# Optimization experiments

Measured on AMD Instinct MI355X. Metric: run time of the kernel, lower is better.

## Reference

```python
import jax, jax.numpy as jnp
import numpy as np


def _tsallis15_probs(x):
    """entmax-1.5 / Tsallis alpha=1.5 mapping over axis=1. x: [n, d] logits."""
    x = (x - jnp.max(x, axis=1, keepdims=True)) * 0.5
    xs = -jnp.sort(-x, axis=1)                       # descending sort  [n, d]
    d = x.shape[1]
    rho = jnp.arange(1, d + 1, dtype=x.dtype)        # 1..d
    mean = jnp.cumsum(xs, axis=1) / rho
    mean_sq = jnp.cumsum(xs * xs, axis=1) / rho
    ss = rho * (mean_sq - mean * mean)
    delta = (1.0 - ss) / rho
    tau = mean - jnp.sqrt(jnp.clip(delta, 0.0))
    support_size = jnp.sum(tau <= xs, axis=1)        # [n]
    tau_star = jnp.take_along_axis(tau, (support_size - 1)[:, None], axis=1)
    y = jnp.clip(x - tau_star, 0.0)
    return y * y                                     # p*, rows sum to 1


def setup_inputs() -> dict:
    key = jax.random.key(0)
    k1, k2 = jax.random.split(key)
    inp = jax.random.normal(k1, (2048, 32000), dtype=jnp.float32)
    target = jax.random.randint(k2, (2048,), 0, 32000, dtype=jnp.int64)
    return {"input": inp, "target": target}


def reference(input, target):
    n = input.shape[0]
    p_star = _tsallis15_probs(input)
    # omega_tsallis15: (1 - sum p^{3/2}) / 0.75 per row
    loss = (1.0 - jnp.sum(p_star * jnp.sqrt(p_star), axis=1)) / 0.75
    # scatter_add(-1) at the target class, then <p* - e_y, x> per row
    pm = p_star.at[jnp.arange(n), target].add(-1.0)
    loss = loss + jnp.einsum('ij,ij->i', pm, input)
    # reduction='elementwise_mean', ignore_index=-100 (<0: no masking)
    return jnp.sum(loss) / n
```

## Files before the change

### kernel.cpp

```cpp
#include <hip/hip_runtime.h>
#include <math.h>

#define BLOCK 512
#define NV 16
#define NWAVES (BLOCK / 64)
#define CAND_CAP 6144
#define NREG 12

__device__ __forceinline__ float waveReduceMax(float v) {
#pragma unroll
    for (int off = 32; off > 0; off >>= 1)
        v = fmaxf(v, __shfl_down(v, off, 64));
    return v;
}
__device__ __forceinline__ float waveReduceSum(float v) {
#pragma unroll
    for (int off = 32; off > 0; off >>= 1)
        v += __shfl_down(v, off, 64);
    return v;
}

__global__ __launch_bounds__(BLOCK, 4) void tsallis15_kernel(
    const float* __restrict__ x, const int* __restrict__ tgt,
    float* __restrict__ out, int n, int d, float inv_n)
{
    __shared__ float s_cand[CAND_CAP];
    __shared__ float s_red[NWAVES];
    __shared__ int   s_cnt;
    __shared__ float s_bcast;

    const int row  = blockIdx.x;
    const int t    = threadIdx.x;
    const int lane = t & 63;
    const int wave = t >> 6;
    const float* __restrict__ xr = x + (size_t)row * (size_t)d;

    if (t == 0) s_cnt = 0;

    float4 r[NV];
#pragma unroll
    for (int i = 0; i < NV; ++i) {
        int e = (i * BLOCK + t) * 4;
        if (e + 4 <= d) {
            r[i] = *reinterpret_cast<const float4*>(xr + e);
        } else {
            float4 v = make_float4(-INFINITY, -INFINITY, -INFINITY, -INFINITY);
            if (e < d)     v.x = xr[e];
            if (e + 1 < d) v.y = xr[e + 1];
            if (e + 2 < d) v.z = xr[e + 2];
            r[i] = v;
        }
    }

    float m = -INFINITY;
#pragma unroll
    for (int i = 0; i < NV; ++i)
        m = fmaxf(m, fmaxf(fmaxf(r[i].x, r[i].y), fmaxf(r[i].z, r[i].w)));
    m = waveReduceMax(m);
    if (lane == 0) s_red[wave] = m;
    __syncthreads();
    if (wave == 0) {
        float v = (lane < NWAVES) ? s_red[lane] : -INFINITY;
        v = waveReduceMax(v);
        if (lane == 0) s_bcast = v;
    }
    __syncthreads();
    const float rowmax = s_bcast;

    const float thr = rowmax - 2.0f;
#pragma unroll
    for (int i = 0; i < NV; ++i) {
        float vals[4] = { r[i].x, r[i].y, r[i].z, r[i].w };
#pragma unroll
        for (int c = 0; c < 4; ++c) {
            float v = vals[c];
            bool pred = (v >= thr);
            unsigned long long mask = __ballot(pred);
            if (mask) {
                int base;
                if (lane == 0) base = atomicAdd(&s_cnt, __popcll(mask));
                base = __shfl(base, 0, 64);
                if (pred) {
                    int pos = base + (int)__popcll(mask & ((1ull << lane) - 1ull));
                    if (pos < CAND_CAP) s_cand[pos] = (v - rowmax) * 0.5f;
                }
            }
        }
    }
    __syncthreads();

    if (wave == 0) {
        const float xt = (lane == 0) ? xr[tgt[row]] : 0.0f;

        const int k = min(s_cnt, CAND_CAP);

        float ur[NREG];
#pragma unroll
        for (int j = 0; j < NREG; ++j) {
            int idx = lane + 64 * j;
            ur[j] = (idx < k) ? s_cand[idx] : -1e30f;
        }

        float lo = -1.0f, hi = 0.0f;
        for (int it = 0; it < 18; ++it) {
            float tau = 0.5f * (lo + hi);
            float acc = 0.0f;
#pragma unroll
            for (int j = 0; j < NREG; ++j) {
                float u = ur[j] - tau;
                acc += (u > 0.0f) ? u * u : 0.0f;
            }
            for (int j = 64 * NREG + lane; j < k; j += 64) {
                float u = s_cand[j] - tau;
                if (u > 0.0f) acc += u * u;
            }
            float tot = waveReduceSum(acc);
            tot = __shfl(tot, 0, 64);
            if (tot >= 1.0f) lo = tau; else hi = tau;
        }
        const float tau_b = 0.5f * (lo + hi);

        float s1 = 0.0f, s2 = 0.0f, sc = 0.0f;
#pragma unroll
        for (int j = 0; j < NREG; ++j) {
            float u = ur[j];
            if (u > tau_b) { s1 += u; s2 += u * u; sc += 1.0f; }
        }
        for (int j = 64 * NREG + lane; j < k; j += 64) {
            float u = s_cand[j];
            if (u > tau_b) { s1 += u; s2 += u * u; sc += 1.0f; }
        }
        s1 = waveReduceSum(s1); s1 = __shfl(s1, 0, 64);
        s2 = waveReduceSum(s2); s2 = __shfl(s2, 0, 64);
        sc = waveReduceSum(sc); sc = __shfl(sc, 0, 64);
        float mean  = s1 / sc;
        float ss    = s2 - s1 * mean;
        float delta = (1.0f - ss) / sc;
        if (delta < 0.0f) delta = 0.0f;
        const float tau_star = mean - sqrtf(delta);

        float p32 = 0.0f, dot = 0.0f;
#pragma unroll
        for (int j = 0; j < NREG; ++j) {
            float u = ur[j] - tau_star;
            if (u > 0.0f) {
                float p = u * u;
                p32 += p * u;
                dot += p * (2.0f * ur[j] + rowmax);
            }
        }
        for (int j = 64 * NREG + lane; j < k; j += 64) {
            float uc = s_cand[j];
            float u  = uc - tau_star;
            if (u > 0.0f) {
                float p = u * u;
                p32 += p * u;
                dot += p * (2.0f * uc + rowmax);
            }
        }
        p32 = waveReduceSum(p32);
        dot = waveReduceSum(dot);
        if (lane == 0) {
            float loss = (1.0f - p32) * (4.0f / 3.0f) + dot - xt;
            atomicAdd(out, loss * inv_n);
        }
    }
}

extern "C" void kernel_launch(void* const* d_in, const int* in_sizes, int n_in,
                              void* d_out, int out_size, void* d_ws, size_t ws_size,
                              hipStream_t stream) {
    const float* x   = (const float*)d_in[0];
    const int*   tgt = (const int*)d_in[1];
    float*       out = (float*)d_out;

    const int n = in_sizes[1];
    const int d = in_sizes[0] / n;

    hipMemsetAsync(out, 0, (size_t)out_size * sizeof(float), stream);
    tsallis15_kernel<<<n, BLOCK, 0, stream>>>(x, tgt, out, n, d, 1.0f / (float)n);
}
```

Measured before the change: 381.1 us.

## Stream row in chunks with per-wave running-max candidate filtering to cut registers

Instead of holding all 64 row values per thread in registers until the block max is known, each wave loads four float4 chunks at a time, tracks a running wave max, and appends values within 2 of it to a per-wave shared segment, pruning the segment when it fills. After the block max is known, the surviving candidates are filtered again into a final list, with a fallback that rereads the row from global memory if any wave's segment overflowed. This lowers register pressure so launch bounds can be raised to 6 blocks per CU. The cost is more shared memory (about 48KB per block, which may itself limit occupancy), extra ballot work, and a possible second global read on overflow.

```diff
diff --git a/kernel.cpp b/kernel.cpp
--- a/kernel.cpp
+++ b/kernel.cpp
@@ -2,15 +2,16 @@
 #include <math.h>
 
 #define BLOCK 512
+#define NWAVES (BLOCK / 64)
 #define NV 16
-#define NWAVES (BLOCK / 64)
-#define CAND_CAP 6144
+#define SEGCAP 1024
+#define FCAP 4096
 #define NREG 12
 
-__device__ __forceinline__ float waveReduceMax(float v) {
-#pragma unroll
-    for (int off = 32; off > 0; off >>= 1)
-        v = fmaxf(v, __shfl_down(v, off, 64));
+__device__ __forceinline__ float waveAllMax(float v) {
+#pragma unroll
+    for (int off = 1; off < 64; off <<= 1)
+        v = fmaxf(v, __shfl_xor(v, off, 64));
     return v;
 }
 __device__ __forceinline__ float waveReduceSum(float v) {
@@ -20,13 +21,32 @@
     return v;
 }
 
-__global__ __launch_bounds__(BLOCK, 4) void tsallis15_kernel(
+__device__ __forceinline__ int wavePrune(float* seg, int cnt, float thr, int lane) {
+    int newcnt = 0;
+    for (int base = 0; base < cnt; base += 64) {
+        int idx = base + lane;
+        bool valid = idx < cnt;
+        float v = valid ? seg[idx] : -INFINITY;
+        bool keep = valid && (v >= thr);
+        unsigned long long mask = __ballot(keep);
+        if (keep) {
+            int pos = newcnt + (int)__popcll(mask & ((1ull << lane) - 1ull));
+            seg[pos] = v;
+        }
+        newcnt += (int)__popcll(mask);
+    }
+    return newcnt;
+}
+
+__global__ __launch_bounds__(BLOCK, 6) void tsallis15_kernel(
     const float* __restrict__ x, const int* __restrict__ tgt,
     float* __restrict__ out, int n, int d, float inv_n)
 {
-    __shared__ float s_cand[CAND_CAP];
+    __shared__ float s_seg[NWAVES][SEGCAP];
+    __shared__ float s_final[FCAP];
     __shared__ float s_red[NWAVES];
-    __shared__ int   s_cnt;
+    __shared__ int   s_fcnt;
+    __shared__ int   s_flag;
     __shared__ float s_bcast;
 
     const int row  = blockIdx.x;
@@ -35,54 +55,114 @@
     const int wave = t >> 6;
     const float* __restrict__ xr = x + (size_t)row * (size_t)d;
 
-    if (t == 0) s_cnt = 0;
-
-    float4 r[NV];
-#pragma unroll
-    for (int i = 0; i < NV; ++i) {
-        int e = (i * BLOCK + t) * 4;
-        if (e + 4 <= d) {
-            r[i] = *reinterpret_cast<const float4*>(xr + e);
-        } else {
-            float4 v = make_float4(-INFINITY, -INFINITY, -INFINITY, -INFINITY);
-            if (e < d)     v.x = xr[e];
-            if (e + 1 < d) v.y = xr[e + 1];
-            if (e + 2 < d) v.z = xr[e + 2];
-            r[i] = v;
-        }
-    }
-
-    float m = -INFINITY;
-#pragma unroll
-    for (int i = 0; i < NV; ++i)
-        m = fmaxf(m, fmaxf(fmaxf(r[i].x, r[i].y), fmaxf(r[i].z, r[i].w)));
-    m = waveReduceMax(m);
-    if (lane == 0) s_red[wave] = m;
+    if (t == 0) { s_fcnt = 0; s_flag = 0; }
+
+    float* seg = &s_seg[wave][0];
+    float wmax = -INFINITY;
+    int   cnt  = 0;
+    bool  ovf  = false;
+
+    for (int i0 = 0; i0 < NV; i0 += 4) {
+        float4 c[4];
+#pragma unroll
+        for (int q = 0; q < 4; ++q) {
+            int e = ((i0 + q) * BLOCK + t) * 4;
+            if (e + 4 <= d) {
+                c[q] = *reinterpret_cast<const float4*>(xr + e);
+            } else {
+                float4 v = make_float4(-INFINITY, -INFINITY, -INFINITY, -INFINITY);
+                if (e < d)     v.x = xr[e];
+                if (e + 1 < d) v.y = xr[e + 1];
+                if (e + 2 < d) v.z = xr[e + 2];
+                c[q] = v;
+            }
+        }
+        float m = -INFINITY;
+#pragma unroll
+        for (int q = 0; q < 4; ++q)
+            m = fmaxf(m, fmaxf(fmaxf(c[q].x, c[q].y), fmaxf(c[q].z, c[q].w)));
+        wmax = fmaxf(wmax, waveAllMax(m));
+        const float thr = wmax - 2.0f;
+#pragma unroll
+        for (int q = 0; q < 4; ++q) {
+            float vals[4] = { c[q].x, c[q].y, c[q].z, c[q].w };
+#pragma unroll
+            for (int s = 0; s < 4; ++s) {
+                float v = vals[s];
+                bool pred = (v >= thr);
+                unsigned long long mask = __ballot(pred);
+                if (mask) {
+                    int pc = (int)__popcll(mask);
+                    if (cnt + pc > SEGCAP) {
+                        cnt = wavePrune(seg, cnt, thr, lane);
+                        if (cnt + pc > SEGCAP) ovf = true;
+                    }
+                    if (!ovf) {
+                        if (pred) {
+                            int pos = cnt + (int)__popcll(mask & ((1ull << lane) - 1ull));
+                            seg[pos] = v;
+                        }
+                        cnt += pc;
+                    }
+                }
+            }
+        }
+    }
+
+    if (lane == 0) {
+        s_red[wave] = wmax;
+        if (ovf) s_flag = 1;
+    }
     __syncthreads();
     if (wave == 0) {
         float v = (lane < NWAVES) ? s_red[lane] : -INFINITY;
-        v = waveReduceMax(v);
+        v = waveAllMax(v);
         if (lane == 0) s_bcast = v;
     }
     __syncthreads();
     const float rowmax = s_bcast;
-
-    const float thr = rowmax - 2.0f;
-#pragma unroll
-    for (int i = 0; i < NV; ++i) {
-        float vals[4] = { r[i].x, r[i].y, r[i].z, r[i].w };
-#pragma unroll
-        for (int c = 0; c < 4; ++c) {
-            float v = vals[c];
-            bool pred = (v >= thr);
-            unsigned long long mask = __ballot(pred);
+    const float thrF   = rowmax - 2.0f;
+
+    if (s_flag == 0) {
+        for (int base = 0; base < cnt; base += 64) {
+            int idx = base + lane;
+            float v = (idx < cnt) ? seg[idx] : -INFINITY;
+            bool keep = (v >= thrF);
+            unsigned long long mask = __ballot(keep);
             if (mask) {
-                int base;
-                if (lane == 0) base = atomicAdd(&s_cnt, __popcll(mask));
-                base = __shfl(base, 0, 64);
-                if (pred) {
-                    int pos = base + (int)__popcll(mask & ((1ull << lane) - 1ull));
-                    if (pos < CAND_CAP) s_cand[pos] = (v - rowmax) * 0.5f;
+                int bpos;
+                if (lane == 0) bpos = atomicAdd(&s_fcnt, (int)__popcll(mask));
+                bpos = __shfl(bpos, 0, 64);
+                if (keep) {
+                    int pos = bpos + (int)__popcll(mask & ((1ull << lane) - 1ull));
+                    if (pos < FCAP) s_final[pos] = (v - rowmax) * 0.5f;
+                }
+            }
+        }
+    } else {
+        for (int i = 0; i < NV; ++i) {
+            int e = (i * BLOCK + t) * 4;
+            float4 c = make_float4(-INFINITY, -INFINITY, -INFINITY, -INFINITY);
+            if (e + 4 <= d) c = *reinterpret_cast<const float4*>(xr + e);
+            else {
+                if (e < d)     c.x = xr[e];
+                if (e + 1 < d) c.y = xr[e + 1];
+                if (e + 2 < d) c.z = xr[e + 2];
+            }
+            float vals[4] = { c.x, c.y, c.z, c.w };
+#pragma unroll
+            for (int s = 0; s < 4; ++s) {
+                float v = vals[s];
+                bool keep = (v >= thrF);
+                unsigned long long mask = __ballot(keep);
+                if (mask) {
+                    int bpos;
+                    if (lane == 0) bpos = atomicAdd(&s_fcnt, (int)__popcll(mask));
+                    bpos = __shfl(bpos, 0, 64);
+                    if (keep) {
+                        int pos = bpos + (int)__popcll(mask & ((1ull << lane) - 1ull));
+                        if (pos < FCAP) s_final[pos] = (v - rowmax) * 0.5f;
+                    }
                 }
             }
         }
@@ -92,13 +172,13 @@
     if (wave == 0) {
         const float xt = (lane == 0) ? xr[tgt[row]] : 0.0f;
 
-        const int k = min(s_cnt, CAND_CAP);
+        const int k = min(s_fcnt, FCAP);
 
         float ur[NREG];
 #pragma unroll
         for (int j = 0; j < NREG; ++j) {
             int idx = lane + 64 * j;
-            ur[j] = (idx < k) ? s_cand[idx] : -1e30f;
+            ur[j] = (idx < k) ? s_final[idx] : -1e30f;
         }
 
         float lo = -1.0f, hi = 0.0f;
@@ -111,7 +191,7 @@
                 acc += (u > 0.0f) ? u * u : 0.0f;
             }
             for (int j = 64 * NREG + lane; j < k; j += 64) {
-                float u = s_cand[j] - tau;
+                float u = s_final[j] - tau;
                 if (u > 0.0f) acc += u * u;
             }
             float tot = waveReduceSum(acc);
@@ -127,7 +207,7 @@
             if (u > tau_b) { s1 += u; s2 += u * u; sc += 1.0f; }
         }
         for (int j = 64 * NREG + lane; j < k; j += 64) {
-            float u = s_cand[j];
+            float u = s_final[j];
             if (u > tau_b) { s1 += u; s2 += u * u; sc += 1.0f; }
         }
         s1 = waveReduceSum(s1); s1 = __shfl(s1, 0, 64);
@@ -150,7 +230,7 @@
             }
         }
         for (int j = 64 * NREG + lane; j < k; j += 64) {
-            float uc = s_cand[j];
+            float uc = s_final[j];
             float u  = uc - tau_star;
             if (u > 0.0f) {
                 float p = u * u;
```

Measured after the change: 384.9 us. Within noise of the previous version (+1.0%).

## Split each row across eight slice blocks with a two-kernel filter and solve

Applied to the files above, without the earlier changes.

Replaces the single one-block-per-row kernel with two kernels. The first uses eight blocks per row; each computes its slice max and writes the values above slicemax-2 to workspace. The second merges the slice candidates against the global row threshold, falling back to a full-row rescan if any slice overflows, and then runs the existing bisection solve. The aim is more blocks and higher occupancy for the memory-bound pass, at the cost of a second launch and workspace traffic.

```diff
diff --git a/kernel.cpp b/kernel.cpp
--- a/kernel.cpp
+++ b/kernel.cpp
@@ -1,11 +1,13 @@
 #include <hip/hip_runtime.h>
 #include <math.h>
 
-#define BLOCK 512
-#define NV 16
-#define NWAVES (BLOCK / 64)
-#define CAND_CAP 6144
-#define NREG 12
+#define SLICES     8
+#define SLICE_CAP  512
+#define K1_BLOCK   256
+#define K2_BLOCK   256
+#define MAXNI      8
+#define FCAP       6144
+#define NREG       12
 
 __device__ __forceinline__ float waveReduceMax(float v) {
 #pragma unroll
@@ -20,69 +22,179 @@
     return v;
 }
 
-__global__ __launch_bounds__(BLOCK, 4) void tsallis15_kernel(
-    const float* __restrict__ x, const int* __restrict__ tgt,
-    float* __restrict__ out, int n, int d, float inv_n)
+__global__ __launch_bounds__(K1_BLOCK, 4) void k1_filter(
+    const float* __restrict__ x, float* __restrict__ cand,
+    int* __restrict__ cnt, float* __restrict__ smax,
+    int d, int slice_len, int ni)
 {
-    __shared__ float s_cand[CAND_CAP];
-    __shared__ float s_red[NWAVES];
+    __shared__ float s_red[K1_BLOCK / 64];
     __shared__ int   s_cnt;
+    __shared__ float s_c[SLICE_CAP];
+    __shared__ float s_bmax;
+
+    const int sid  = blockIdx.x;
+    const int row  = sid >> 3;
+    const int sl   = sid & 7;
+    const int t    = threadIdx.x;
+    const int lane = t & 63;
+    const int wave = t >> 6;
+
+    if (t == 0) s_cnt = 0;
+
+    const int sbeg = sl * slice_len;
+    const int send = min(sbeg + slice_len, d);
+    const float* __restrict__ xr = x + (size_t)row * (size_t)d;
+
+    float4 c[MAXNI];
+#pragma unroll
+    for (int i = 0; i < MAXNI; ++i)
+        c[i] = make_float4(-INFINITY, -INFINITY, -INFINITY, -INFINITY);
+
+    float m = -INFINITY;
+    for (int i = 0; i < ni; ++i) {
+        int p = sbeg + (i * K1_BLOCK + t) * 4;
+        float4 v = make_float4(-INFINITY, -INFINITY, -INFINITY, -INFINITY);
+        if (p + 4 <= send) {
+            v = *reinterpret_cast<const float4*>(xr + p);
+        } else if (p < send) {
+            v.x = xr[p];
+            if (p + 1 < send) v.y = xr[p + 1];
+            if (p + 2 < send) v.z = xr[p + 2];
+        }
+        if (i < MAXNI) c[i] = v;
+        m = fmaxf(m, fmaxf(fmaxf(v.x, v.y), fmaxf(v.z, v.w)));
+    }
+    m = waveReduceMax(m);
+    if (lane == 0) s_red[wave] = m;
+    __syncthreads();
+    if (t == 0) {
+        float v = s_red[0];
+#pragma unroll
+        for (int w = 1; w < K1_BLOCK / 64; ++w) v = fmaxf(v, s_red[w]);
+        s_bmax = v;
+    }
+    __syncthreads();
+    const float mx  = s_bmax;
+    const float thr = mx - 2.0f;
+
+    for (int i = 0; i < ni; ++i) {
+        float4 v;
+        if (i < MAXNI) {
+            v = c[i];
+        } else {
+            int p = sbeg + (i * K1_BLOCK + t) * 4;
+            v = make_float4(-INFINITY, -INFINITY, -INFINITY, -INFINITY);
+            if (p + 4 <= send) v = *reinterpret_cast<const float4*>(xr + p);
+            else if (p < send) {
+                v.x = xr[p];
+                if (p + 1 < send) v.y = xr[p + 1];
+                if (p + 2 < send) v.z = xr[p + 2];
+            }
+        }
+        float vals[4] = { v.x, v.y, v.z, v.w };
+#pragma unroll
+        for (int s = 0; s < 4; ++s) {
+            float w = vals[s];
+            bool pred = (w >= thr);
+            unsigned long long mask = __ballot(pred);
+            if (mask) {
+                int base;
+                if (lane == 0) base = atomicAdd(&s_cnt, (int)__popcll(mask));
+                base = __shfl(base, 0, 64);
+                if (pred) {
+                    int pos = base + (int)__popcll(mask & ((1ull << lane) - 1ull));
+                    if (pos < SLICE_CAP) s_c[pos] = w;
+                }
+            }
+        }
+    }
+    __syncthreads();
+
+    const int total = s_cnt;
+    if (t == 0) { cnt[sid] = total; smax[sid] = mx; }
+    const int wr = min(total, SLICE_CAP);
+    for (int j = t; j < wr; j += K1_BLOCK)
+        cand[(size_t)sid * SLICE_CAP + j] = s_c[j];
+}
+
+__global__ __launch_bounds__(K2_BLOCK, 4) void k2_solve(
+    const float* __restrict__ x, const float* __restrict__ cand,
+    const int* __restrict__ cnt, const float* __restrict__ smax,
+    const int* __restrict__ tgt, float* __restrict__ out,
+    int d, float inv_n)
+{
+    __shared__ float s_final[FCAP];
+    __shared__ int   s_cnt8[SLICES];
+    __shared__ int   s_fcnt;
+    __shared__ int   s_ovf;
     __shared__ float s_bcast;
 
     const int row  = blockIdx.x;
     const int t    = threadIdx.x;
     const int lane = t & 63;
     const int wave = t >> 6;
+
+    if (t == 0) { s_fcnt = 0; s_ovf = 0; }
+
+    if (wave == 0) {
+        float v = -INFINITY;
+        if (lane < SLICES) {
+            int c8 = cnt[row * SLICES + lane];
+            s_cnt8[lane] = min(c8, SLICE_CAP);
+            if (c8 > SLICE_CAP) s_ovf = 1;
+            v = smax[row * SLICES + lane];
+        }
+#pragma unroll
+        for (int off = 1; off < SLICES; off <<= 1)
+            v = fmaxf(v, __shfl_xor(v, off, 64));
+        if (lane == 0) s_bcast = v;
+    }
+    __syncthreads();
+    const float rowmax = s_bcast;
+    const float thr    = rowmax - 2.0f;
     const float* __restrict__ xr = x + (size_t)row * (size_t)d;
 
-    if (t == 0) s_cnt = 0;
-
-    float4 r[NV];
-#pragma unroll
-    for (int i = 0; i < NV; ++i) {
-        int e = (i * BLOCK + t) * 4;
-        if (e + 4 <= d) {
-            r[i] = *reinterpret_cast<const float4*>(xr + e);
-        } else {
-            float4 v = make_float4(-INFINITY, -INFINITY, -INFINITY, -INFINITY);
-            if (e < d)     v.x = xr[e];
-            if (e + 1 < d) v.y = xr[e + 1];
-            if (e + 2 < d) v.z = xr[e + 2];
-            r[i] = v;
-        }
-    }
-
-    float m = -INFINITY;
-#pragma unroll
-    for (int i = 0; i < NV; ++i)
-        m = fmaxf(m, fmaxf(fmaxf(r[i].x, r[i].y), fmaxf(r[i].z, r[i].w)));
-    m = waveReduceMax(m);
-    if (lane == 0) s_red[wave] = m;
-    __syncthreads();
-    if (wave == 0) {
-        float v = (lane < NWAVES) ? s_red[lane] : -INFINITY;
-        v = waveReduceMax(v);
-        if (lane == 0) s_bcast = v;
-    }
-    __syncthreads();
-    const float rowmax = s_bcast;
-
-    const float thr = rowmax - 2.0f;
-#pragma unroll
-    for (int i = 0; i < NV; ++i) {
-        float vals[4] = { r[i].x, r[i].y, r[i].z, r[i].w };
-#pragma unroll
-        for (int c = 0; c < 4; ++c) {
-            float v = vals[c];
-            bool pred = (v >= thr);
-            unsigned long long mask = __ballot(pred);
+    if (!s_ovf) {
+        const float* __restrict__ cr = cand + (size_t)row * SLICES * SLICE_CAP;
+        for (int j = t; j < SLICES * SLICE_CAP; j += K2_BLOCK) {
+            int slice = j >> 9;
+            int pos   = j & (SLICE_CAP - 1);
+            float v   = cr[j];
+            bool keep = (pos < s_cnt8[slice]) && (v >= thr);
+            unsigned long long mask = __ballot(keep);
             if (mask) {
                 int base;
-                if (lane == 0) base = atomicAdd(&s_cnt, __popcll(mask));
+                if (lane == 0) base = atomicAdd(&s_fcnt, (int)__popcll(mask));
                 base = __shfl(base, 0, 64);
-                if (pred) {
-                    int pos = base + (int)__popcll(mask & ((1ull << lane) - 1ull));
-                    if (pos < CAND_CAP) s_cand[pos] = (v - rowmax) * 0.5f;
+                if (keep) {
+                    int p2 = base + (int)__popcll(mask & ((1ull << lane) - 1ull));
+                    if (p2 < FCAP) s_final[p2] = (v - rowmax) * 0.5f;
+                }
+            }
+        }
+    } else {
+        for (int e0 = t * 4; e0 < d; e0 += K2_BLOCK * 4) {
+            float4 v = make_float4(-INFINITY, -INFINITY, -INFINITY, -INFINITY);
+            if (e0 + 4 <= d) v = *reinterpret_cast<const float4*>(xr + e0);
+            else {
+                v.x = xr[e0];
+                if (e0 + 1 < d) v.y = xr[e0 + 1];
+                if (e0 + 2 < d) v.z = xr[e0 + 2];
+            }
+            float vals[4] = { v.x, v.y, v.z, v.w };
+#pragma unroll
+            for (int s = 0; s < 4; ++s) {
+                float w = vals[s];
+                bool keep = (w >= thr);
+                unsigned long long mask = __ballot(keep);
+                if (mask) {
+                    int base;
+                    if (lane == 0) base = atomicAdd(&s_fcnt, (int)__popcll(mask));
+                    base = __shfl(base, 0, 64);
+                    if (keep) {
+                        int p2 = base + (int)__popcll(mask & ((1ull << lane) - 1ull));
+                        if (p2 < FCAP) s_final[p2] = (w - rowmax) * 0.5f;
+                    }
                 }
             }
         }
@@ -92,13 +204,13 @@
     if (wave == 0) {
         const float xt = (lane == 0) ? xr[tgt[row]] : 0.0f;
 
-        const int k = min(s_cnt, CAND_CAP);
+        const int k = min(s_fcnt, FCAP);
 
         float ur[NREG];
 #pragma unroll
         for (int j = 0; j < NREG; ++j) {
             int idx = lane + 64 * j;
-            ur[j] = (idx < k) ? s_cand[idx] : -1e30f;
+            ur[j] = (idx < k) ? s_final[idx] : -1e30f;
         }
 
         float lo = -1.0f, hi = 0.0f;
@@ -111,7 +223,7 @@
                 acc += (u > 0.0f) ? u * u : 0.0f;
             }
             for (int j = 64 * NREG + lane; j < k; j += 64) {
-                float u = s_cand[j] - tau;
+                float u = s_final[j] - tau;
                 if (u > 0.0f) acc += u * u;
             }
             float tot = waveReduceSum(acc);
@@ -127,7 +239,7 @@
             if (u > tau_b) { s1 += u; s2 += u * u; sc += 1.0f; }
         }
         for (int j = 64 * NREG + lane; j < k; j += 64) {
-            float u = s_cand[j];
+            float u = s_final[j];
             if (u > tau_b) { s1 += u; s2 += u * u; sc += 1.0f; }
         }
         s1 = waveReduceSum(s1); s1 = __shfl(s1, 0, 64);
@@ -150,7 +262,7 @@
             }
         }
         for (int j = 64 * NREG + lane; j < k; j += 64) {
-            float uc = s_cand[j];
+            float uc = s_final[j];
             float u  = uc - tau_star;
             if (u > 0.0f) {
                 float p = u * u;
@@ -177,6 +289,14 @@
     const int n = in_sizes[1];
     const int d = in_sizes[0] / n;
 
+    const int slice_len = ((d + 4 * SLICES - 1) / (4 * SLICES)) * 4;
+    const int ni        = (slice_len + K1_BLOCK * 4 - 1) / (K1_BLOCK * 4);
+
+    float* cand = (float*)d_ws;
+    int*   cnt  = (int*)((char*)d_ws + (size_t)n * SLICES * SLICE_CAP * sizeof(float));
+    float* smax = (float*)((char*)cnt + (size_t)n * SLICES * sizeof(int));
+
     hipMemsetAsync(out, 0, (size_t)out_size * sizeof(float), stream);
-    tsallis15_kernel<<<n, BLOCK, 0, stream>>>(x, tgt, out, n, d, 1.0f / (float)n);
-}
+    k1_filter<<<n * SLICES, K1_BLOCK, 0, stream>>>(x, cand, cnt, smax, d, slice_len, ni);
+    k2_solve<<<n, K2_BLOCK, 0, stream>>>(x, cand, cnt, smax, tgt, out, d, 1.0f / (float)n);
+}
```

New measurement: 552.3 us. 1.45x slower.
